# Kernel tuning notes

Measured on AMD Instinct MI355X. Metric: run time of the kernel, lower is better.

Reference implementation:

```python
import jax, jax.numpy as jnp
import numpy as np

CLASSES = (32, 32)
SUPERCLASSES = 8
OVERALL = CLASSES[0] * CLASSES[1]
CLASS_FACTOR = OVERALL // SUPERCLASSES


def lrelu(x):
    return jax.nn.leaky_relu(x, 0.01)


def conv1x1(x, w, b):
    # x: [B,C,H,W], w: [O,C], b: [O]
    return jnp.einsum('oc,bchw->bohw', w, x) + b[None, :, None, None]


def cond_mul(x, inds, W, b):
    # x: [N,I], inds: [N] int, W: [K,I,O], b: [K,O]
    return jnp.einsum('ni,nio->no', x, W[inds]) + b[inds]


def setup_inputs() -> dict:
    key = jax.random.key(0)
    ks = jax.random.split(key, 24)
    s = 0.05
    d = {}
    d['x_in'] = jax.random.normal(ks[0], (1, 128, 192, 256), dtype=jnp.float32)
    # mask branch
    d['Wm1'] = jax.random.normal(ks[1], (32, 128)) * s
    d['bm1'] = jnp.zeros((32,), jnp.float32)
    d['Wm2'] = jax.random.normal(ks[2], (16, 32)) * s
    d['bm2'] = jnp.zeros((16,), jnp.float32)
    d['Wm3'] = jax.random.normal(ks[3], (1, 16)) * s
    d['bm3'] = jnp.zeros((1,), jnp.float32)
    # classification branch
    d['Wcl1'] = jax.random.normal(ks[4], (128, 128)) * s
    d['bcl1'] = jnp.zeros((128,), jnp.float32)
    d['Wcl21'] = jax.random.normal(ks[5], (128, 128)) * s
    d['bcl21'] = jnp.zeros((128,), jnp.float32)
    d['Wcl31'] = jax.random.normal(ks[6], (32, 128)) * s
    d['bcl31'] = jnp.zeros((32,), jnp.float32)
    d['Wcl22'] = jax.random.normal(ks[7], (CLASSES[0], 128, 32)) * s  # CondMul
    d['bcl22'] = jnp.zeros((CLASSES[0], 32), jnp.float32)
    d['Wcl32'] = jax.random.normal(ks[8], (CLASSES[0], 32, CLASSES[1])) * s
    d['bcl32'] = jnp.zeros((CLASSES[0], CLASSES[1]), jnp.float32)
    d['Wr1'] = jax.random.normal(ks[9], (128, 128)) * s
    d['br1'] = jnp.zeros((128,), jnp.float32)
    d['Wr2'] = jax.random.normal(ks[10], (SUPERCLASSES, 128, 32)) * s
    d['br2'] = jnp.zeros((SUPERCLASSES, 32), jnp.float32)
    d['Wr3'] = jax.random.normal(ks[11], (OVERALL, 32, 1)) * s
    d['br3'] = jnp.zeros((OVERALL, 1), jnp.float32)
    return d


def reference(x_in, Wm1, bm1, Wm2, bm2, Wm3, bm3,
              Wcl1, bcl1, Wcl21, bcl21, Wcl31, bcl31,
              Wcl22, bcl22, Wcl32, bcl32,
              Wr1, br1, Wr2, br2, Wr3, br3):
    B = x_in.shape[0]
    # mask branch
    m = lrelu(conv1x1(x_in, Wm1, bm1))
    m = lrelu(conv1x1(m, Wm2, bm2))
    mask = lrelu(conv1x1(m, Wm3, bm3))
    # classification branch
    x = lrelu(conv1x1(x_in, Wcl1, bcl1))          # [B,128,H,W]
    # torch: transpose(1,3) -> [B,W,H,C], flatten
    x_l = jnp.transpose(x, (0, 3, 2, 1)).reshape(-1, x.shape[1])
    x2 = lrelu(conv1x1(x, Wcl21, bcl21))
    cl1 = conv1x1(x2, Wcl31, bcl31)               # [B,classes0,H,W]
    inds1 = jnp.argmax(cl1, axis=1).reshape(-1).astype(jnp.int32)  # [N] (B,H,W order)
    h = lrelu(cond_mul(x_l, inds1, Wcl22, bcl22))  # [N,32]
    h = cond_mul(h, inds1, Wcl32, bcl32)           # [N,classes1]
    inds2 = jnp.argmax(h, axis=1).astype(jnp.int32)
    inds = inds1 * CLASSES[1] + inds2
    inds_r = jnp.clip(inds, 0, OVERALL - 1).astype(jnp.int32)
    inds_super = jnp.clip(inds_r // CLASS_FACTOR, 0, SUPERCLASSES - 1)
    r = lrelu(conv1x1(x_in, Wr1, br1))
    r_l = jnp.transpose(r, (0, 3, 2, 1)).reshape(-1, r.shape[1])
    r2 = lrelu(cond_mul(r_l, inds_super, Wr2, br2))  # [N,32]
    regression = cond_mul(r2, inds_r, Wr3, br3)      # [N,1]
    regression = regression.reshape(B, 1, 1, -1)
    inds = inds.reshape(regression.shape)
    x_real = (inds.astype(jnp.float32) + regression) * (1.0 / float(OVERALL))
    return (x_real, mask)
```

## Files before the change

### kernel.cpp

```cpp
#include <hip/hip_runtime.h>

#define HH 192
#define WW 256
#define NPIX (HH*WW)
#define NSEG (NPIX/64)

__device__ __forceinline__ float lrelu(float v) { return v > 0.0f ? v : 0.01f * v; }

__global__ __launch_bounds__(256, 3) void k_fused1(
    const float* __restrict__ X,
    const float* __restrict__ Wcl1, const float* __restrict__ bcl1,
    const float* __restrict__ Wr1,  const float* __restrict__ br1,
    const float* __restrict__ Wm1,  const float* __restrict__ bm1,
    const float* __restrict__ Wm2,  const float* __restrict__ bm2,
    const float* __restrict__ Wm3,  const float* __restrict__ bm3,
    float* __restrict__ x_t, float* __restrict__ r_t,
    float* __restrict__ out)
{
    __shared__ float As[16][132];
    __shared__ float Ws[16][132];
    __shared__ float m1buf[128][33];
    const int tid = threadIdx.x;
    const int q0  = blockIdx.x * 128;

    if (blockIdx.y == 2) {
        const int tc = tid & 31;
        const int tr = tid >> 5;
        float acc[4][4];
        #pragma unroll
        for (int i = 0; i < 4; ++i)
            #pragma unroll
            for (int j = 0; j < 4; ++j)
                acc[i][j] = bm1[tr * 4 + j];

        for (int k0 = 0; k0 < 128; k0 += 16) {
            #pragma unroll
            for (int p = 0; p < 2; ++p) {
                int lin = p * 1024 + tid * 4;
                int kk = lin >> 7, px = lin & 127;
                float4 v = *(const float4*)(X + (k0 + kk) * NPIX + q0 + px);
                *(float4*)(&As[kk][px]) = v;
            }
            if (tid < 128) {
                int row = tid >> 2, kc = (tid & 3) * 4;
                float4 v = *(const float4*)(Wm1 + row * 128 + k0 + kc);
                Ws[kc + 0][row] = v.x; Ws[kc + 1][row] = v.y;
                Ws[kc + 2][row] = v.z; Ws[kc + 3][row] = v.w;
            }
            __syncthreads();
            #pragma unroll
            for (int kk = 0; kk < 16; ++kk) {
                float4 a = *(const float4*)(&As[kk][tc * 4]);
                float4 w = *(const float4*)(&Ws[kk][tr * 4]);
                float av[4] = {a.x,a.y,a.z,a.w};
                float wv[4] = {w.x,w.y,w.z,w.w};
                #pragma unroll
                for (int i = 0; i < 4; ++i)
                    #pragma unroll
                    for (int j = 0; j < 4; ++j)
                        acc[i][j] = fmaf(av[i], wv[j], acc[i][j]);
            }
            __syncthreads();
        }
        #pragma unroll
        for (int i = 0; i < 4; ++i)
            #pragma unroll
            for (int j = 0; j < 4; ++j)
                m1buf[tc * 4 + i][tr * 4 + j] = lrelu(acc[i][j]);
        __syncthreads();
        if (tid < 128) {
            float m3 = bm3[0];
            #pragma unroll 2
            for (int j = 0; j < 16; ++j) {
                float s = bm2[j];
                #pragma unroll
                for (int k = 0; k < 32; ++k)
                    s = fmaf(Wm2[j * 32 + k], m1buf[tid][k], s);
                m3 = fmaf(Wm3[j], lrelu(s), m3);
            }
            out[NPIX + q0 + tid] = lrelu(m3);
        }
        return;
    }

    const float* __restrict__ W    = (blockIdx.y == 0) ? Wcl1 : Wr1;
    const float* __restrict__ bias = (blockIdx.y == 0) ? bcl1 : br1;
    float* __restrict__ outp       = (blockIdx.y == 0) ? x_t : r_t;

    const int tc = tid & 15;
    const int tr = tid >> 4;

    float acc[8][8];
    #pragma unroll
    for (int i = 0; i < 8; ++i)
        #pragma unroll
        for (int j = 0; j < 8; ++j)
            acc[i][j] = bias[(j >> 2) * 64 + tr * 4 + (j & 3)];

    for (int k0 = 0; k0 < 128; k0 += 16) {
        #pragma unroll
        for (int p = 0; p < 2; ++p) {
            int lin = p * 1024 + tid * 4;
            int kk = lin >> 7, px = lin & 127;
            float4 v = *(const float4*)(X + (k0 + kk) * NPIX + q0 + px);
            *(float4*)(&As[kk][px]) = v;
        }
        #pragma unroll
        for (int p = 0; p < 2; ++p) {
            int lin = p * 1024 + tid * 4;
            int row = lin >> 4, kc = lin & 15;
            float4 v = *(const float4*)(W + row * 128 + k0 + kc);
            Ws[kc + 0][row] = v.x; Ws[kc + 1][row] = v.y;
            Ws[kc + 2][row] = v.z; Ws[kc + 3][row] = v.w;
        }
        __syncthreads();
        #pragma unroll
        for (int kk = 0; kk < 16; ++kk) {
            float4 a0 = *(const float4*)(&As[kk][tc * 4]);
            float4 a1 = *(const float4*)(&As[kk][64 + tc * 4]);
            float4 w0 = *(const float4*)(&Ws[kk][tr * 4]);
            float4 w1 = *(const float4*)(&Ws[kk][64 + tr * 4]);
            float av[8] = {a0.x,a0.y,a0.z,a0.w,a1.x,a1.y,a1.z,a1.w};
            float wv[8] = {w0.x,w0.y,w0.z,w0.w,w1.x,w1.y,w1.z,w1.w};
            #pragma unroll
            for (int i = 0; i < 8; ++i)
                #pragma unroll
                for (int j = 0; j < 8; ++j)
                    acc[i][j] = fmaf(av[i], wv[j], acc[i][j]);
        }
        __syncthreads();
    }

    #pragma unroll
    for (int i = 0; i < 8; ++i) {
        int px = (i >> 2) * 64 + tc * 4 + (i & 3);
        int q  = q0 + px;
        int np = (q & 255) * 192 + (q >> 8);
        float* op = outp + (size_t)np * 128;
        #pragma unroll
        for (int jg = 0; jg < 2; ++jg) {
            float4 o;
            o.x = lrelu(acc[i][jg*4+0]); o.y = lrelu(acc[i][jg*4+1]);
            o.z = lrelu(acc[i][jg*4+2]); o.w = lrelu(acc[i][jg*4+3]);
            *(float4*)(op + jg * 64 + tr * 4) = o;
        }
    }
}

__global__ __launch_bounds__(256, 2) void k1b(
    const float* __restrict__ x_t,
    const float* __restrict__ Wcl21, const float* __restrict__ bcl21,
    const float* __restrict__ Wcl31, const float* __restrict__ bcl31,
    int* __restrict__ inds1_q)
{
    __shared__ float smem[12672];
    float (*As)[132]     = (float(*)[132])smem;
    float (*Ws)[132]     = (float(*)[132])(smem + 2112);
    float (*W31)[132]    = (float(*)[132])smem;
    float (*x2t)[132]    = (float(*)[132])(smem + 4224);
    float (*cl1buf)[33]  = (float(*)[33]) (smem + 4224);

    const int tid = threadIdx.x;
    const int n0  = blockIdx.x * 128;
    const int tcA = tid & 15, trA = tid >> 4;
    const int tcB = tid & 31, trB = tid >> 5;

    float accB[4][4];
    #pragma unroll
    for (int i = 0; i < 4; ++i)
        #pragma unroll
        for (int j = 0; j < 4; ++j)
            accB[i][j] = bcl31[trB * 4 + j];

    for (int h = 0; h < 2; ++h) {
        float acc2[2][4][4];
        #pragma unroll
        for (int gi = 0; gi < 2; ++gi)
            #pragma unroll
            for (int i = 0; i < 4; ++i)
                #pragma unroll
                for (int j = 0; j < 4; ++j)
                    acc2[gi][i][j] = bcl21[h * 64 + trA * 4 + j];

        for (int k0 = 0; k0 < 128; k0 += 16) {
            #pragma unroll
            for (int p = 0; p < 2; ++p) {
                int lin = p * 1024 + tid * 4;
                int px = lin >> 4, kc = lin & 15;
                float4 v = *(const float4*)(x_t + (size_t)(n0 + px) * 128 + k0 + kc);
                As[kc + 0][px] = v.x; As[kc + 1][px] = v.y;
                As[kc + 2][px] = v.z; As[kc + 3][px] = v.w;
            }
            {
                int r = tid >> 2, kc = (tid & 3) * 4;
                float4 v = *(const float4*)(Wcl21 + (h * 64 + r) * 128 + k0 + kc);
                Ws[kc + 0][r] = v.x; Ws[kc + 1][r] = v.y;
                Ws[kc + 2][r] = v.z; Ws[kc + 3][r] = v.w;
            }
            __syncthreads();
            #pragma unroll
            for (int kk = 0; kk < 16; ++kk) {
                float4 a0 = *(const float4*)(&As[kk][tcA * 4]);
                float4 a1 = *(const float4*)(&As[kk][64 + tcA * 4]);
                float4 w  = *(const float4*)(&Ws[kk][trA * 4]);
                float av0[4] = {a0.x,a0.y,a0.z,a0.w};
                float av1[4] = {a1.x,a1.y,a1.z,a1.w};
                float wv[4]  = {w.x,w.y,w.z,w.w};
                #pragma unroll
                for (int i = 0; i < 4; ++i)
                    #pragma unroll
                    for (int j = 0; j < 4; ++j) {
                        acc2[0][i][j] = fmaf(av0[i], wv[j], acc2[0][i][j]);
                        acc2[1][i][j] = fmaf(av1[i], wv[j], acc2[1][i][j]);
                    }
            }
            __syncthreads();
        }
        #pragma unroll
        for (int j = 0; j < 4; ++j) {
            int row = trA * 4 + j;
            #pragma unroll
            for (int gi = 0; gi < 2; ++gi) {
                float4 o;
                o.x = lrelu(acc2[gi][0][j]); o.y = lrelu(acc2[gi][1][j]);
                o.z = lrelu(acc2[gi][2][j]); o.w = lrelu(acc2[gi][3][j]);
                *(float4*)(&x2t[row][gi * 64 + tcA * 4]) = o;
            }
        }
        __syncthreads();
        #pragma unroll
        for (int p = 0; p < 4; ++p) {
            int lin = p * 1024 + tid * 4;
            int row = lin >> 7, kc = lin & 127;
            *(float4*)(&W31[row][kc]) = *(const float4*)(Wcl31 + row * 128 + kc);
        }
        __syncthreads();
        for (int k = 0; k < 64; ++k) {
            float4 a = *(const float4*)(&x2t[k][tcB * 4]);
            float av[4] = {a.x,a.y,a.z,a.w};
            float wv[4];
            #pragma unroll
            for (int j = 0; j < 4; ++j) wv[j] = W31[trB * 4 + j][h * 64 + k];
            #pragma unroll
            for (int i = 0; i < 4; ++i)
                #pragma unroll
                for (int j = 0; j < 4; ++j)
                    accB[i][j] = fmaf(av[i], wv[j], accB[i][j]);
        }
        __syncthreads();
    }

    #pragma unroll
    for (int i = 0; i < 4; ++i)
        #pragma unroll
        for (int j = 0; j < 4; ++j)
            cl1buf[tcB * 4 + i][trB * 4 + j] = accB[i][j];
    __syncthreads();
    if (tid < 128) {
        float bv = cl1buf[tid][0]; int bi = 0;
        #pragma unroll
        for (int c = 1; c < 32; ++c) {
            float v = cl1buf[tid][c];
            if (v > bv) { bv = v; bi = c; }
        }
        int n = n0 + tid;
        int w = n / 192, hh = n - w * 192;
        inds1_q[hh * 256 + w] = bi;
    }
}

__global__ void k_hist(const int* __restrict__ inds1_q, int* __restrict__ bh) {
    int tid = threadIdx.x;
    int n = blockIdx.x * 256 + tid;
    int key = inds1_q[n];
    int lane = tid & 63;
    int cnt = 0;
    for (int k = 0; k < 32; ++k) {
        unsigned long long m = __ballot(key == k);
        if (lane == k) cnt = __popcll(m);
    }
    if (lane < 32) bh[(n >> 6) * 32 + lane] = cnt;
}

__global__ void k_scanA(const int* __restrict__ bh, int* __restrict__ ebb,
                        int* __restrict__ total) {
    __shared__ int s[256];
    const int k = blockIdx.x, t = threadIdx.x;
    int v0 = bh[(t * 3 + 0) * 32 + k];
    int v1 = bh[(t * 3 + 1) * 32 + k];
    int v2 = bh[(t * 3 + 2) * 32 + k];
    int sum = v0 + v1 + v2;
    s[t] = sum; __syncthreads();
    for (int d = 1; d < 256; d <<= 1) {
        int x = (t >= d) ? s[t - d] : 0;
        __syncthreads();
        s[t] += x;
        __syncthreads();
    }
    int ex = s[t] - sum;
    ebb[(t * 3 + 0) * 32 + k] = ex;
    ebb[(t * 3 + 1) * 32 + k] = ex + v0;
    ebb[(t * 3 + 2) * 32 + k] = ex + v0 + v1;
    if (t == 255) total[k] = s[255];
}

__global__ void k_scatter2(const int* __restrict__ inds1_q,
                           const int* __restrict__ ebb,
                           const int* __restrict__ total,
                           int* __restrict__ order)
{
    __shared__ int ttot[32];
    const int tid = threadIdx.x;
    if (tid < 32) ttot[tid] = total[tid];
    __syncthreads();
    int n = blockIdx.x * 256 + tid;
    int key = inds1_q[n];
    int lane = tid & 63;
    unsigned long long peers = 0;
    for (int k = 0; k < 32; ++k) {
        unsigned long long m = __ballot(key == k);
        if (key == k) peers = m;
    }
    int rank = __popcll(peers & ((1ull << lane) - 1ull));
    int cbase = 0;
    #pragma unroll
    for (int k = 0; k < 32; ++k) cbase += (k < key) ? ttot[k] : 0;
    order[cbase + ebb[(n >> 6) * 32 + key] + rank] = n;
}

__global__ __launch_bounds__(256, 4) void k2h(
    const float* __restrict__ x_t,
    const float* __restrict__ Wcl22, const float* __restrict__ bcl22,
    const float* __restrict__ Wcl32, const float* __restrict__ bcl32,
    const int* __restrict__ total, const int* __restrict__ order,
    int* __restrict__ ind_ord)
{
    __shared__ float Was[4096];
    __shared__ float Wbs[1024];
    __shared__ int cpre[33];
    __shared__ int cbase[33];
    __shared__ int ttot[32];

    const int tid = threadIdx.x;
    if (tid < 32) ttot[tid] = total[tid];
    __syncthreads();
    if (tid == 0) {
        int s = 0, cb = 0;
        for (int k = 0; k < 32; ++k) {
            cpre[k] = s; cbase[k] = cb;
            int c = ttot[k];
            s += (c + 255) >> 8;
            cb += c;
        }
        cpre[32] = s; cbase[32] = cb;
    }
    __syncthreads();
    const int ci = blockIdx.x;
    if (ci >= cpre[32]) return;
    int cls = 0;
    while (cpre[cls + 1] <= ci) ++cls;
    const int st   = (ci - cpre[cls]) * 256;
    const int npx  = min(256, ttot[cls] - st);
    const int base = cbase[cls] + st;

    {
        const float4* ws = (const float4*)(Wcl22 + cls * 4096);
        #pragma unroll
        for (int j = 0; j < 4; ++j) ((float4*)Was)[j * 256 + tid] = ws[j * 256 + tid];
        ((float4*)Wbs)[tid] = ((const float4*)(Wcl32 + cls * 1024))[tid];
    }
    __syncthreads();

    const int m = order[base + min(tid, npx - 1)];
    const float4* xp = (const float4*)(x_t + (size_t)m * 128);

    float h[32];
    #pragma unroll
    for (int j = 0; j < 32; ++j) h[j] = bcl22[cls * 32 + j];
    #pragma unroll 2
    for (int c4 = 0; c4 < 32; ++c4) {
        float4 xv = xp[c4];
        float xa[4] = {xv.x, xv.y, xv.z, xv.w};
        #pragma unroll
        for (int cc = 0; cc < 4; ++cc) {
            const float* wr = &Was[(c4 * 4 + cc) * 32];
            #pragma unroll
            for (int j = 0; j < 32; ++j) h[j] = fmaf(xa[cc], wr[j], h[j]);
        }
    }
    #pragma unroll
    for (int j = 0; j < 32; ++j) h[j] = lrelu(h[j]);

    float g[32];
    #pragma unroll
    for (int j = 0; j < 32; ++j) g[j] = bcl32[cls * 32 + j];
    #pragma unroll 2
    for (int c = 0; c < 32; ++c) {
        float hv = h[c];
        const float* wr = &Wbs[c * 32];
        #pragma unroll
        for (int j = 0; j < 32; ++j) g[j] = fmaf(hv, wr[j], g[j]);
    }
    float bv = g[0]; int bi = 0;
    #pragma unroll
    for (int j = 1; j < 32; ++j)
        if (g[j] > bv) { bv = g[j]; bi = j; }
    if (tid < npx) ind_ord[base + tid] = cls * 32 + bi;
}

__global__ __launch_bounds__(256, 4) void k2r(
    const float* __restrict__ r_t,
    const float* __restrict__ Wr2,  const float* __restrict__ br2,
    const float* __restrict__ Wr3,  const float* __restrict__ br3,
    const int* __restrict__ total, const int* __restrict__ order,
    const int* __restrict__ ind_ord,
    float* __restrict__ out)
{
    __shared__ float Wcs[4096];
    __shared__ int cpre[33];
    __shared__ int cbase[33];
    __shared__ int ttot[32];

    const int tid = threadIdx.x;
    if (tid < 32) ttot[tid] = total[tid];
    __syncthreads();
    if (tid == 0) {
        int s = 0, cb = 0;
        for (int k = 0; k < 32; ++k) {
            cpre[k] = s; cbase[k] = cb;
            int c = ttot[k];
            s += (c + 255) >> 8;
            cb += c;
        }
        cpre[32] = s; cbase[32] = cb;
    }
    __syncthreads();
    const int ci = blockIdx.x;
    if (ci >= cpre[32]) return;
    int cls = 0;
    while (cpre[cls + 1] <= ci) ++cls;
    const int st   = (ci - cpre[cls]) * 256;
    const int npx  = min(256, ttot[cls] - st);
    const int base = cbase[cls] + st;
    const int sup  = cls >> 2;

    {
        const float4* ws = (const float4*)(Wr2 + sup * 4096);
        #pragma unroll
        for (int j = 0; j < 4; ++j) ((float4*)Wcs)[j * 256 + tid] = ws[j * 256 + tid];
    }
    __syncthreads();

    const int li  = min(tid, npx - 1);
    const int m   = order[base + li];
    const int ind = ind_ord[base + li];
    const float4* rp = (const float4*)(r_t + (size_t)m * 128);

    float r2[32];
    #pragma unroll
    for (int j = 0; j < 32; ++j) r2[j] = br2[sup * 32 + j];
    #pragma unroll 2
    for (int c4 = 0; c4 < 32; ++c4) {
        float4 rv = rp[c4];
        float ra[4] = {rv.x, rv.y, rv.z, rv.w};
        #pragma unroll
        for (int cc = 0; cc < 4; ++cc) {
            const float* wr = &Wcs[(c4 * 4 + cc) * 32];
            #pragma unroll
            for (int j = 0; j < 32; ++j) r2[j] = fmaf(ra[cc], wr[j], r2[j]);
        }
    }

    float reg = br3[ind];
    const float* __restrict__ w3 = Wr3 + ind * 32;
    #pragma unroll
    for (int j = 0; j < 32; ++j) reg = fmaf(lrelu(r2[j]), w3[j], reg);

    if (tid < npx) out[m] = ((float)ind + reg) * (1.0f / 1024.0f);
}

extern "C" void kernel_launch(void* const* d_in, const int* in_sizes, int n_in,
                              void* d_out, int out_size, void* d_ws, size_t ws_size,
                              hipStream_t stream)
{
    const float* X     = (const float*)d_in[0];
    const float* Wm1   = (const float*)d_in[1];
    const float* bm1   = (const float*)d_in[2];
    const float* Wm2   = (const float*)d_in[3];
    const float* bm2   = (const float*)d_in[4];
    const float* Wm3   = (const float*)d_in[5];
    const float* bm3   = (const float*)d_in[6];
    const float* Wcl1  = (const float*)d_in[7];
    const float* bcl1  = (const float*)d_in[8];
    const float* Wcl21 = (const float*)d_in[9];
    const float* bcl21 = (const float*)d_in[10];
    const float* Wcl31 = (const float*)d_in[11];
    const float* bcl31 = (const float*)d_in[12];
    const float* Wcl22 = (const float*)d_in[13];
    const float* bcl22 = (const float*)d_in[14];
    const float* Wcl32 = (const float*)d_in[15];
    const float* bcl32 = (const float*)d_in[16];
    const float* Wr1   = (const float*)d_in[17];
    const float* br1   = (const float*)d_in[18];
    const float* Wr2   = (const float*)d_in[19];
    const float* br2   = (const float*)d_in[20];
    const float* Wr3   = (const float*)d_in[21];
    const float* br3   = (const float*)d_in[22];
    float* out = (float*)d_out;

    float* x_t   = (float*)d_ws;
    float* r_t   = x_t + (size_t)NPIX * 128;
    int* inds1_q = (int*)(r_t + (size_t)NPIX * 128);
    int* order   = inds1_q + NPIX;
    int* ind_ord = order + NPIX;
    int* bh      = ind_ord + NPIX;
    int* ebb     = bh + NSEG * 32;
    int* total   = ebb + NSEG * 32;

    k_fused1<<<dim3(NPIX / 128, 3), 256, 0, stream>>>(X, Wcl1, bcl1, Wr1, br1,
                                                      Wm1, bm1, Wm2, bm2, Wm3, bm3,
                                                      x_t, r_t, out);
    k1b<<<NPIX / 128, 256, 0, stream>>>(x_t, Wcl21, bcl21, Wcl31, bcl31, inds1_q);
    k_hist<<<NPIX / 256, 256, 0, stream>>>(inds1_q, bh);
    k_scanA<<<32, 256, 0, stream>>>(bh, ebb, total);
    k_scatter2<<<NPIX / 256, 256, 0, stream>>>(inds1_q, ebb, total, order);
    k2h<<<224, 256, 0, stream>>>(x_t, Wcl22, bcl22, Wcl32, bcl32, total, order, ind_ord);
    k2r<<<224, 256, 0, stream>>>(r_t, Wr2, br2, Wr3, br3, total, order, ind_ord, out);
}
```

Baseline: 247.7 us.

## Prefetch GEMM tiles into registers and fuse k2h/k2r into one kernel

Adds register double-buffering to the k_fused1 and k1b GEMM loops, so the next K-slice's global loads are issued before the current slice's FMAs and written to shared memory afterwards. Raises launch-bounds occupancy targets for both kernels. Merges the classification and regression cond-mul kernels into one, which removes a launch and the ind_ord round trip through global memory. The extra prefetch registers and higher occupancy targets may cause spills, and the fused kernel uses more shared memory per block.

```diff
diff --git a/kernel.cpp b/kernel.cpp
--- a/kernel.cpp
+++ b/kernel.cpp
@@ -7,7 +7,7 @@
 
 __device__ __forceinline__ float lrelu(float v) { return v > 0.0f ? v : 0.01f * v; }
 
-__global__ __launch_bounds__(256, 3) void k_fused1(
+__global__ __launch_bounds__(256, 4) void k_fused1(
     const float* __restrict__ X,
     const float* __restrict__ Wcl1, const float* __restrict__ bcl1,
     const float* __restrict__ Wr1,  const float* __restrict__ br1,
@@ -97,23 +97,33 @@
         for (int j = 0; j < 8; ++j)
             acc[i][j] = bias[(j >> 2) * 64 + tr * 4 + (j & 3)];
 
+    float4 pa[2], pw[2];
+    #pragma unroll
+    for (int p = 0; p < 2; ++p) {
+        int lin = p * 1024 + tid * 4;
+        pa[p] = *(const float4*)(X + (lin >> 7) * NPIX + q0 + (lin & 127));
+        pw[p] = *(const float4*)(W + (lin >> 4) * 128 + (lin & 15));
+    }
+    #pragma unroll
+    for (int p = 0; p < 2; ++p) {
+        int lin = p * 1024 + tid * 4;
+        *(float4*)(&As[lin >> 7][lin & 127]) = pa[p];
+        int row = lin >> 4, kc = lin & 15;
+        Ws[kc + 0][row] = pw[p].x; Ws[kc + 1][row] = pw[p].y;
+        Ws[kc + 2][row] = pw[p].z; Ws[kc + 3][row] = pw[p].w;
+    }
+    __syncthreads();
+
     for (int k0 = 0; k0 < 128; k0 += 16) {
-        #pragma unroll
-        for (int p = 0; p < 2; ++p) {
-            int lin = p * 1024 + tid * 4;
-            int kk = lin >> 7, px = lin & 127;
-            float4 v = *(const float4*)(X + (k0 + kk) * NPIX + q0 + px);
-            *(float4*)(&As[kk][px]) = v;
-        }
-        #pragma unroll
-        for (int p = 0; p < 2; ++p) {
-            int lin = p * 1024 + tid * 4;
-            int row = lin >> 4, kc = lin & 15;
-            float4 v = *(const float4*)(W + row * 128 + k0 + kc);
-            Ws[kc + 0][row] = v.x; Ws[kc + 1][row] = v.y;
-            Ws[kc + 2][row] = v.z; Ws[kc + 3][row] = v.w;
-        }
-        __syncthreads();
+        const bool more = (k0 + 16) < 128;
+        if (more) {
+            #pragma unroll
+            for (int p = 0; p < 2; ++p) {
+                int lin = p * 1024 + tid * 4;
+                pa[p] = *(const float4*)(X + (k0 + 16 + (lin >> 7)) * NPIX + q0 + (lin & 127));
+                pw[p] = *(const float4*)(W + (lin >> 4) * 128 + k0 + 16 + (lin & 15));
+            }
+        }
         #pragma unroll
         for (int kk = 0; kk < 16; ++kk) {
             float4 a0 = *(const float4*)(&As[kk][tc * 4]);
@@ -129,6 +139,17 @@
                     acc[i][j] = fmaf(av[i], wv[j], acc[i][j]);
         }
         __syncthreads();
+        if (more) {
+            #pragma unroll
+            for (int p = 0; p < 2; ++p) {
+                int lin = p * 1024 + tid * 4;
+                *(float4*)(&As[lin >> 7][lin & 127]) = pa[p];
+                int row = lin >> 4, kc = lin & 15;
+                Ws[kc + 0][row] = pw[p].x; Ws[kc + 1][row] = pw[p].y;
+                Ws[kc + 2][row] = pw[p].z; Ws[kc + 3][row] = pw[p].w;
+            }
+        }
+        __syncthreads();
     }
 
     #pragma unroll
@@ -147,7 +168,7 @@
     }
 }
 
-__global__ __launch_bounds__(256, 2) void k1b(
+__global__ __launch_bounds__(256, 3) void k1b(
     const float* __restrict__ x_t,
     const float* __restrict__ Wcl21, const float* __restrict__ bcl21,
     const float* __restrict__ Wcl31, const float* __restrict__ bcl31,
@@ -182,22 +203,37 @@
                 for (int j = 0; j < 4; ++j)
                     acc2[gi][i][j] = bcl21[h * 64 + trA * 4 + j];
 
+        float4 pa[2], pw;
+        #pragma unroll
+        for (int p = 0; p < 2; ++p) {
+            int lin = p * 1024 + tid * 4;
+            pa[p] = *(const float4*)(x_t + (size_t)(n0 + (lin >> 4)) * 128 + (lin & 15));
+        }
+        pw = *(const float4*)(Wcl21 + (h * 64 + (tid >> 2)) * 128 + (tid & 3) * 4);
+        #pragma unroll
+        for (int p = 0; p < 2; ++p) {
+            int lin = p * 1024 + tid * 4;
+            int px = lin >> 4, kc = lin & 15;
+            As[kc + 0][px] = pa[p].x; As[kc + 1][px] = pa[p].y;
+            As[kc + 2][px] = pa[p].z; As[kc + 3][px] = pa[p].w;
+        }
+        {
+            int r = tid >> 2, kc = (tid & 3) * 4;
+            Ws[kc + 0][r] = pw.x; Ws[kc + 1][r] = pw.y;
+            Ws[kc + 2][r] = pw.z; Ws[kc + 3][r] = pw.w;
+        }
+        __syncthreads();
+
         for (int k0 = 0; k0 < 128; k0 += 16) {
-            #pragma unroll
-            for (int p = 0; p < 2; ++p) {
-                int lin = p * 1024 + tid * 4;
-                int px = lin >> 4, kc = lin & 15;
-                float4 v = *(const float4*)(x_t + (size_t)(n0 + px) * 128 + k0 + kc);
-                As[kc + 0][px] = v.x; As[kc + 1][px] = v.y;
-                As[kc + 2][px] = v.z; As[kc + 3][px] = v.w;
-            }
-            {
-                int r = tid >> 2, kc = (tid & 3) * 4;
-                float4 v = *(const float4*)(Wcl21 + (h * 64 + r) * 128 + k0 + kc);
-                Ws[kc + 0][r] = v.x; Ws[kc + 1][r] = v.y;
-                Ws[kc + 2][r] = v.z; Ws[kc + 3][r] = v.w;
-            }
-            __syncthreads();
+            const bool more = (k0 + 16) < 128;
+            if (more) {
+                #pragma unroll
+                for (int p = 0; p < 2; ++p) {
+                    int lin = p * 1024 + tid * 4;
+                    pa[p] = *(const float4*)(x_t + (size_t)(n0 + (lin >> 4)) * 128 + k0 + 16 + (lin & 15));
+                }
+                pw = *(const float4*)(Wcl21 + (h * 64 + (tid >> 2)) * 128 + k0 + 16 + (tid & 3) * 4);
+            }
             #pragma unroll
             for (int kk = 0; kk < 16; ++kk) {
                 float4 a0 = *(const float4*)(&As[kk][tcA * 4]);
@@ -213,6 +249,19 @@
                         acc2[0][i][j] = fmaf(av0[i], wv[j], acc2[0][i][j]);
                         acc2[1][i][j] = fmaf(av1[i], wv[j], acc2[1][i][j]);
                     }
+            }
+            __syncthreads();
+            if (more) {
+                #pragma unroll
+                for (int p = 0; p < 2; ++p) {
+                    int lin = p * 1024 + tid * 4;
+                    int px = lin >> 4, kc = lin & 15;
+                    As[kc + 0][px] = pa[p].x; As[kc + 1][px] = pa[p].y;
+                    As[kc + 2][px] = pa[p].z; As[kc + 3][px] = pa[p].w;
+                }
+                int r = tid >> 2, kc = (tid & 3) * 4;
+                Ws[kc + 0][r] = pw.x; Ws[kc + 1][r] = pw.y;
+                Ws[kc + 2][r] = pw.z; Ws[kc + 3][r] = pw.w;
             }
             __syncthreads();
         }
@@ -328,15 +377,18 @@
     order[cbase + ebb[(n >> 6) * 32 + key] + rank] = n;
 }
 
-__global__ __launch_bounds__(256, 4) void k2h(
-    const float* __restrict__ x_t,
+__global__ __launch_bounds__(256, 4) void k2(
+    const float* __restrict__ x_t, const float* __restrict__ r_t,
     const float* __restrict__ Wcl22, const float* __restrict__ bcl22,
     const float* __restrict__ Wcl32, const float* __restrict__ bcl32,
+    const float* __restrict__ Wr2,  const float* __restrict__ br2,
+    const float* __restrict__ Wr3,  const float* __restrict__ br3,
     const int* __restrict__ total, const int* __restrict__ order,
-    int* __restrict__ ind_ord)
+    float* __restrict__ out)
 {
     __shared__ float Was[4096];
     __shared__ float Wbs[1024];
+    __shared__ float Wcs[4096];
     __shared__ int cpre[33];
     __shared__ int cbase[33];
     __shared__ int ttot[32];
@@ -362,18 +414,24 @@
     const int st   = (ci - cpre[cls]) * 256;
     const int npx  = min(256, ttot[cls] - st);
     const int base = cbase[cls] + st;
+    const int sup  = cls >> 2;
 
     {
-        const float4* ws = (const float4*)(Wcl22 + cls * 4096);
-        #pragma unroll
-        for (int j = 0; j < 4; ++j) ((float4*)Was)[j * 256 + tid] = ws[j * 256 + tid];
+        const float4* wa = (const float4*)(Wcl22 + cls * 4096);
+        const float4* wc = (const float4*)(Wr2 + sup * 4096);
+        #pragma unroll
+        for (int j = 0; j < 4; ++j) {
+            ((float4*)Was)[j * 256 + tid] = wa[j * 256 + tid];
+            ((float4*)Wcs)[j * 256 + tid] = wc[j * 256 + tid];
+        }
         ((float4*)Wbs)[tid] = ((const float4*)(Wcl32 + cls * 1024))[tid];
     }
     __syncthreads();
 
-    const int m = order[base + min(tid, npx - 1)];
+    const int li = min(tid, npx - 1);
+    const int m  = order[base + li];
+
     const float4* xp = (const float4*)(x_t + (size_t)m * 128);
-
     float h[32];
     #pragma unroll
     for (int j = 0; j < 32; ++j) h[j] = bcl22[cls * 32 + j];
@@ -405,57 +463,9 @@
     #pragma unroll
     for (int j = 1; j < 32; ++j)
         if (g[j] > bv) { bv = g[j]; bi = j; }
-    if (tid < npx) ind_ord[base + tid] = cls * 32 + bi;
-}
-
-__global__ __launch_bounds__(256, 4) void k2r(
-    const float* __restrict__ r_t,
-    const float* __restrict__ Wr2,  const float* __restrict__ br2,
-    const float* __restrict__ Wr3,  const float* __restrict__ br3,
-    const int* __restrict__ total, const int* __restrict__ order,
-    const int* __restrict__ ind_ord,
-    float* __restrict__ out)
-{
-    __shared__ float Wcs[4096];
-    __shared__ int cpre[33];
-    __shared__ int cbase[33];
-    __shared__ int ttot[32];
-
-    const int tid = threadIdx.x;
-    if (tid < 32) ttot[tid] = total[tid];
-    __syncthreads();
-    if (tid == 0) {
-        int s = 0, cb = 0;
-        for (int k = 0; k < 32; ++k) {
-            cpre[k] = s; cbase[k] = cb;
-            int c = ttot[k];
-            s += (c + 255) >> 8;
-            cb += c;
-        }
-        cpre[32] = s; cbase[32] = cb;
-    }
-    __syncthreads();
-    const int ci = blockIdx.x;
-    if (ci >= cpre[32]) return;
-    int cls = 0;
-    while (cpre[cls + 1] <= ci) ++cls;
-    const int st   = (ci - cpre[cls]) * 256;
-    const int npx  = min(256, ttot[cls] - st);
-    const int base = cbase[cls] + st;
-    const int sup  = cls >> 2;
-
-    {
-        const float4* ws = (const float4*)(Wr2 + sup * 4096);
-        #pragma unroll
-        for (int j = 0; j < 4; ++j) ((float4*)Wcs)[j * 256 + tid] = ws[j * 256 + tid];
-    }
-    __syncthreads();
-
-    const int li  = min(tid, npx - 1);
-    const int m   = order[base + li];
-    const int ind = ind_ord[base + li];
+    const int ind = cls * 32 + bi;
+
     const float4* rp = (const float4*)(r_t + (size_t)m * 128);
-
     float r2[32];
     #pragma unroll
     for (int j = 0; j < 32; ++j) r2[j] = br2[sup * 32 + j];
@@ -512,8 +522,7 @@
     float* r_t   = x_t + (size_t)NPIX * 128;
     int* inds1_q = (int*)(r_t + (size_t)NPIX * 128);
     int* order   = inds1_q + NPIX;
-    int* ind_ord = order + NPIX;
-    int* bh      = ind_ord + NPIX;
+    int* bh      = order + NPIX;
     int* ebb     = bh + NSEG * 32;
     int* total   = ebb + NSEG * 32;
 
@@ -524,6 +533,6 @@
     k_hist<<<NPIX / 256, 256, 0, stream>>>(inds1_q, bh);
     k_scanA<<<32, 256, 0, stream>>>(bh, ebb, total);
     k_scatter2<<<NPIX / 256, 256, 0, stream>>>(inds1_q, ebb, total, order);
-    k2h<<<224, 256, 0, stream>>>(x_t, Wcl22, bcl22, Wcl32, bcl32, total, order, ind_ord);
-    k2r<<<224, 256, 0, stream>>>(r_t, Wr2, br2, Wr3, br3, total, order, ind_ord, out);
-}
+    k2<<<224, 256, 0, stream>>>(x_t, r_t, Wcl22, bcl22, Wcl32, bcl32,
+                                Wr2, br2, Wr3, br3, total, order, out);
+}
```

Result: slower. 887.7 us (+258.3%).
